# Optimization experiments

Measured on AMD Instinct MI355X. Metric: run time of the kernel, lower is better.

Reference implementation:

```python
import jax, jax.numpy as jnp
import numpy as np

POOL = 7          # cf.pool_size
SR = 2            # roi_align sampling_ratio
LEVELS = [0, 1, 2, 3]
C = 192           # cf.end_filts
HC = 2            # cf.head_classes
RF = 1
N_ROIS = 1000
B = 4


def roi_align_2d(fmap, boxes, batch_inds, pool_size=POOL, sr=SR):
    """Bilinear RoIAlign. fmap [B,C,H,W]; boxes [N,4] = (y1,x1,y2,x2) in fmap pixel coords."""
    _, _, H, W = fmap.shape
    y1, x1, y2, x2 = boxes[:, 0], boxes[:, 1], boxes[:, 2], boxes[:, 3]
    bin_h = jnp.maximum(y2 - y1, 1.0) / pool_size
    bin_w = jnp.maximum(x2 - x1, 1.0) / pool_size
    # sampling offsets within the roi, [pool*sr]
    grid = (jnp.arange(pool_size, dtype=jnp.float32)[:, None]
            + (jnp.arange(sr, dtype=jnp.float32)[None, :] + 0.5) / sr).reshape(-1)
    ys = y1[:, None] + grid[None, :] * bin_h[:, None]   # [N, P*S]
    xs = x1[:, None] + grid[None, :] * bin_w[:, None]   # [N, P*S]
    y = jnp.broadcast_to(ys[:, :, None], (ys.shape[0], ys.shape[1], xs.shape[1]))  # [N,PS,PS]
    x = jnp.broadcast_to(xs[:, None, :], y.shape)
    valid = (y >= -1.0) & (y <= H) & (x >= -1.0) & (x <= W)
    y = jnp.clip(y, 0.0, H - 1)
    x = jnp.clip(x, 0.0, W - 1)
    y0 = jnp.floor(y).astype(jnp.int32)
    x0 = jnp.floor(x).astype(jnp.int32)
    y1i = jnp.minimum(y0 + 1, H - 1)
    x1i = jnp.minimum(x0 + 1, W - 1)
    ly = y - y0
    lx = x - x0
    b = batch_inds[:, None, None]
    f00 = fmap[b, :, y0, x0]    # [N,PS,PS,C]
    f01 = fmap[b, :, y0, x1i]
    f10 = fmap[b, :, y1i, x0]
    f11 = fmap[b, :, y1i, x1i]
    w00 = ((1 - ly) * (1 - lx))[..., None]
    w01 = ((1 - ly) * lx)[..., None]
    w10 = (ly * (1 - lx))[..., None]
    w11 = (ly * lx)[..., None]
    val = (f00 * w00 + f01 * w01 + f10 * w10 + f11 * w11) * valid[..., None]
    n = val.shape[0]
    val = val.reshape(n, pool_size, sr, pool_size, sr, -1).mean(axis=(2, 4))  # [N,P,P,C]
    return jnp.transpose(val, (0, 3, 1, 2))  # [N,C,P,P]


def pyramid_roi_align(fmaps, rois, pool_size=POOL, levels=LEVELS):
    boxes = jax.lax.stop_gradient(rois[:, :4])  # level_boxes.detach() in original
    batch_ix = rois[:, 4].astype(jnp.int32)
    h = boxes[:, 2] - boxes[:, 0]
    w = boxes[:, 3] - boxes[:, 1]
    roi_level = jnp.clip(jnp.round(4.0 + jnp.log2(jnp.sqrt(h * w))),
                         levels[0], levels[-1]).astype(jnp.int32)
    pooled = jnp.zeros((boxes.shape[0], fmaps[0].shape[1], pool_size, pool_size), fmaps[0].dtype)
    for li, lvl in enumerate(levels):
        H, W = fmaps[li].shape[2], fmaps[li].shape[3]
        scale = jnp.asarray([H, W, H, W], jnp.float32)
        p = roi_align_2d(fmaps[li], boxes * scale, batch_ix, pool_size)
        pooled = jnp.where((roi_level == lvl)[:, None, None, None], p, pooled)
    return pooled


def setup_inputs() -> dict:
    key = jax.random.key(0)
    ks = jax.random.split(key, 20)
    fmap0 = jax.random.normal(ks[0], (B, C, 128, 128), jnp.float32)
    fmap1 = jax.random.normal(ks[1], (B, C, 64, 64), jnp.float32)
    fmap2 = jax.random.normal(ks[2], (B, C, 32, 32), jnp.float32)
    fmap3 = jax.random.normal(ks[3], (B, C, 16, 16), jnp.float32)
    # valid normalized rois: (y1,x1,y2,x2,batch_ix)
    cy = jax.random.uniform(ks[4], (N_ROIS,), minval=0.15, maxval=0.85)
    cx = jax.random.uniform(ks[5], (N_ROIS,), minval=0.15, maxval=0.85)
    hh = jax.random.uniform(ks[6], (N_ROIS,), minval=0.02, maxval=0.15)
    hw = jax.random.uniform(ks[7], (N_ROIS,), minval=0.02, maxval=0.15)
    bix = jax.random.randint(ks[8], (N_ROIS,), 0, B).astype(jnp.float32)
    rois = jnp.stack([jnp.clip(cy - hh, 0, 1), jnp.clip(cx - hw, 0, 1),
                      jnp.clip(cy + hh, 0, 1), jnp.clip(cx + hw, 0, 1), bix], axis=1)
    d = C * 4  # 768
    s1 = 1.0 / np.sqrt(C * POOL * POOL)
    s2 = 1.0 / np.sqrt(d)
    params = dict(
        w1=jax.random.normal(ks[9], (d, C, POOL, POOL), jnp.float32) * s1,
        b1=jnp.zeros((d,), jnp.float32),
        w2=jax.random.normal(ks[10], (d, d), jnp.float32) * s2,
        b2=jnp.zeros((d,), jnp.float32),
        w_bbox=jax.random.normal(ks[11], (HC * 4, d), jnp.float32) * s2,
        b_bbox=jnp.zeros((HC * 4,), jnp.float32),
        w_cls=jax.random.normal(ks[12], (HC, d), jnp.float32) * s2,
        b_cls=jnp.zeros((HC,), jnp.float32),
        w_reg=jax.random.normal(ks[13], (HC * RF, d), jnp.float32) * s2,
        b_reg=jnp.zeros((HC * RF,), jnp.float32),
        w_unc=jax.random.normal(ks[14], (HC, d), jnp.float32) * s2,
        b_unc=jnp.zeros((HC,), jnp.float32),
    )
    return dict(fmap0=fmap0, fmap1=fmap1, fmap2=fmap2, fmap3=fmap3, rois=rois, **params)


def reference(fmap0, fmap1, fmap2, fmap3, rois, w1, b1, w2, b2,
              w_bbox, b_bbox, w_cls, b_cls, w_reg, b_reg, w_unc, b_unc):
    x = pyramid_roi_align([fmap0, fmap1, fmap2, fmap3], rois)      # [N,C,7,7]
    x = jax.nn.relu(jnp.einsum('ncij,ocij->no', x, w1) + b1)       # conv1 ks=7 -> 1x1
    x = jax.nn.relu(x @ w2.T + b2)                                 # conv2 1x1
    n = x.shape[0]
    mrcnn_bbox = (x @ w_bbox.T + b_bbox).reshape(n, -1, 4)         # [N,HC,2*dim]
    mrcnn_class_logits = x @ w_cls.T + b_cls                       # [N,HC]
    reg = (x @ w_reg.T + b_reg).reshape(n, -1, RF)
    unc = x @ w_unc.T + b_unc
    mrcnn_regress = jnp.concatenate([reg, unc[..., None]], axis=2)  # [N,HC,RF+1]
    return mrcnn_bbox, mrcnn_class_logits, mrcnn_regress
```

## Files before the change

### kernel.cpp

```cpp
#include <hip/hip_runtime.h>
#include <hip/hip_bf16.h>
#include <cstddef>
#include <cstdint>

typedef __attribute__((ext_vector_type(8))) short short8;
typedef __attribute__((ext_vector_type(16))) float float16;

#define C_CH 192
#define PK   9408
#define D1   768

__device__ __forceinline__ ushort f2bf(float v) {
    return __builtin_bit_cast(unsigned short, __float2bfloat16(v));
}
__device__ __forceinline__ float bf2f(ushort u) {
    return __builtin_bit_cast(float, ((unsigned int)u) << 16);
}

__global__ __launch_bounds__(256) void cvt_bf16_2(
    const float* __restrict__ in1, ushort* __restrict__ out1, int n4_1,
    const float* __restrict__ in2, ushort* __restrict__ out2, int n4_2)
{
    int i = blockIdx.x * 256 + threadIdx.x;
    const float* in; ushort* out;
    if (i < n4_1) { in = in1; out = out1; }
    else          { i -= n4_1; if (i >= n4_2) return; in = in2; out = out2; }
    float4 v = ((const float4*)in)[i];
    ushort4 o;
    o.x = f2bf(v.x); o.y = f2bf(v.y); o.z = f2bf(v.z); o.w = f2bf(v.w);
    ((ushort4*)out)[i] = o;
}

__global__ __launch_bounds__(256) void cvt_bf16(const float* __restrict__ in,
                                                ushort* __restrict__ out, int n4)
{
    int i = blockIdx.x * 256 + threadIdx.x;
    if (i >= n4) return;
    float4 v = ((const float4*)in)[i];
    ushort4 o;
    o.x = f2bf(v.x); o.y = f2bf(v.y); o.z = f2bf(v.z); o.w = f2bf(v.w);
    ((ushort4*)out)[i] = o;
}

__global__ __launch_bounds__(256) void nchw_to_nhwc(
    const float* __restrict__ f0, const float* __restrict__ f1,
    const float* __restrict__ f2, const float* __restrict__ f3,
    ushort* __restrict__ o0, ushort* __restrict__ o1,
    ushort* __restrict__ o2, ushort* __restrict__ o3)
{
    __shared__ float sm[C_CH][33];
    int t = blockIdx.x;
    int b = blockIdx.y;
    const float* in; ushort* out; int HW, hw0;
    if      (t < 512) { in = f0; out = o0; HW = 16384; hw0 = t * 32; }
    else if (t < 640) { in = f1; out = o1; HW = 4096;  hw0 = (t - 512) * 32; }
    else if (t < 672) { in = f2; out = o2; HW = 1024;  hw0 = (t - 640) * 32; }
    else              { in = f3; out = o3; HW = 256;   hw0 = (t - 672) * 32; }

    int tx = threadIdx.x & 31;
    int ty = threadIdx.x >> 5;

    const float* ip = in + (size_t)b * C_CH * HW + hw0;
    #pragma unroll
    for (int c = 0; c < C_CH; c += 8)
        sm[c + ty][tx] = ip[(size_t)(c + ty) * HW + tx];
    __syncthreads();

    ushort* op = out + ((size_t)b * HW + hw0) * C_CH;
    #pragma unroll
    for (int r0 = 0; r0 < 32; r0 += 8) {
        int r = r0 + ty;
        #pragma unroll
        for (int cc = 0; cc < 6; ++cc) {
            int c = cc * 32 + tx;
            op[(size_t)r * C_CH + c] = f2bf(sm[c][r]);
        }
    }
}

__global__ __launch_bounds__(384) void roi_gather(
    const ushort* __restrict__ n0p, const ushort* __restrict__ n1p,
    const ushort* __restrict__ n2p, const ushort* __restrict__ n3p,
    const float* __restrict__ rois, ushort* __restrict__ pooled)
{
    __shared__ int   s_offB[196][4];
    __shared__ float s_w[196][4];
    __shared__ ushort s_out[PK];

    const int n   = blockIdx.x;
    const int tid = threadIdx.x;

    float by1 = rois[n*5+0], bx1 = rois[n*5+1];
    float by2 = rois[n*5+2], bx2 = rois[n*5+3];
    int   b   = (int)rois[n*5+4];

    float hh = by2 - by1, ww = bx2 - bx1;
    int lvl = (int)rintf(4.0f + log2f(sqrtf(hh * ww)));
    lvl = min(max(lvl, 0), 3);

    const ushort* fm; int H;
    if      (lvl == 0) { fm = n0p; H = 128; }
    else if (lvl == 1) { fm = n1p; H = 64;  }
    else if (lvl == 2) { fm = n2p; H = 32;  }
    else               { fm = n3p; H = 16;  }
    float Hf = (float)H;

    float y1p = by1 * Hf, x1p = bx1 * Hf;
    float y2p = by2 * Hf, x2p = bx2 * Hf;
    float bin_h = fmaxf(y2p - y1p, 1.0f) * (1.0f / 7.0f);
    float bin_w = fmaxf(x2p - x1p, 1.0f) * (1.0f / 7.0f);

    uintptr_t bp = (uintptr_t)(fm + (size_t)b * H * H * C_CH);
    unsigned int blo = __builtin_amdgcn_readfirstlane((unsigned int)bp);
    unsigned int bhi = __builtin_amdgcn_readfirstlane((unsigned int)(bp >> 32));
    const char* sbase = (const char*)((((uintptr_t)bhi) << 32) | blo);

    if (tid < 196) {
        int s  = tid;
        int sx = s & 1, sy = (s >> 1) & 1, ij = s >> 2;
        int i = ij / 7, j = ij - i * 7;

        float gy = (float)i + 0.25f + 0.5f * (float)sy;
        float y  = y1p + gy * bin_h;
        bool  vy = (y >= -1.0f) && (y <= Hf);
        float yc = fminf(fmaxf(y, 0.0f), Hf - 1.0f);
        int   y0 = (int)floorf(yc);
        float ly = yc - (float)y0;
        int   y1i = min(y0 + 1, H - 1);

        float gx = (float)j + 0.25f + 0.5f * (float)sx;
        float x  = x1p + gx * bin_w;
        bool  vx = (x >= -1.0f) && (x <= Hf);
        float xc = fminf(fmaxf(x, 0.0f), Hf - 1.0f);
        int   x0 = (int)floorf(xc);
        float lx = xc - (float)x0;
        int   x1i = min(x0 + 1, H - 1);

        float vm = (vy && vx) ? 0.25f : 0.0f;
        s_offB[s][0] = (y0  * H + x0 ) * (C_CH * 2);
        s_offB[s][1] = (y0  * H + x1i) * (C_CH * 2);
        s_offB[s][2] = (y1i * H + x0 ) * (C_CH * 2);
        s_offB[s][3] = (y1i * H + x1i) * (C_CH * 2);
        s_w[s][0] = (1.0f - ly) * (1.0f - lx) * vm;
        s_w[s][1] = (1.0f - ly) * lx * vm;
        s_w[s][2] = ly * (1.0f - lx) * vm;
        s_w[s][3] = ly * lx * vm;
    }
    __syncthreads();

    const int grp = tid / 96;
    const int ci  = tid - grp * 96;
    const int c   = ci * 2;
    const int c4  = ci * 4;
    const int bin_lo = grp * 13;
    const int bin_hi = min(bin_lo + 13, 49);

    for (int bin = bin_lo; bin < bin_hi; ++bin) {
        float a0 = 0.0f, a1 = 0.0f;
        #pragma unroll
        for (int sub = 0; sub < 4; ++sub) {
            int s = bin * 4 + sub;
            #pragma unroll
            for (int tp = 0; tp < 4; ++tp) {
                int ob  = s_offB[s][tp];
                float w = s_w[s][tp];
                unsigned int u = *(const unsigned int*)(sbase + (ob + c4));
                float lo = __builtin_bit_cast(float, u << 16);
                float hi = __builtin_bit_cast(float, u & 0xffff0000u);
                a0 = fmaf(lo, w, a0);
                a1 = fmaf(hi, w, a1);
            }
        }
        s_out[(c + 0) * 49 + bin] = f2bf(a0);
        s_out[(c + 1) * 49 + bin] = f2bf(a1);
    }
    __syncthreads();

    unsigned int* po = (unsigned int*)(pooled + (size_t)n * PK);
    const unsigned int* so = (const unsigned int*)s_out;
    for (int idx = tid; idx < PK / 2; idx += 384) po[idx] = so[idx];
}

__global__ __launch_bounds__(256) void roi_align_nchw(
    const float* __restrict__ f0, const float* __restrict__ f1,
    const float* __restrict__ f2, const float* __restrict__ f3,
    const float* __restrict__ rois, ushort* __restrict__ pooled, int n_rois)
{
    int idx = blockIdx.x * 256 + threadIdx.x;
    if (idx >= n_rois * PK) return;
    int n  = idx / PK;
    int r  = idx - n * PK;
    int c  = r / 49;
    int ij = r - c * 49;
    int i  = ij / 7;
    int j  = ij - i * 7;

    float by1 = rois[n*5+0], bx1 = rois[n*5+1];
    float by2 = rois[n*5+2], bx2 = rois[n*5+3];
    int   b   = (int)rois[n*5+4];

    float hh = by2 - by1, ww = bx2 - bx1;
    int lvl = (int)rintf(4.0f + log2f(sqrtf(hh * ww)));
    lvl = min(max(lvl, 0), 3);

    const float* fmap; int H;
    if      (lvl == 0) { fmap = f0; H = 128; }
    else if (lvl == 1) { fmap = f1; H = 64;  }
    else if (lvl == 2) { fmap = f2; H = 32;  }
    else               { fmap = f3; H = 16;  }
    float Hf = (float)H;

    float y1p = by1 * Hf, x1p = bx1 * Hf;
    float bin_h = fmaxf(by2 * Hf - y1p, 1.0f) * (1.0f / 7.0f);
    float bin_w = fmaxf(bx2 * Hf - x1p, 1.0f) * (1.0f / 7.0f);

    const float* base = fmap + ((size_t)b * C_CH + c) * (size_t)(H * H);

    float acc = 0.0f;
    #pragma unroll
    for (int sy = 0; sy < 2; ++sy) {
        float y  = y1p + ((float)i + 0.25f + 0.5f * (float)sy) * bin_h;
        bool  vy = (y >= -1.0f) && (y <= Hf);
        float yc = fminf(fmaxf(y, 0.0f), Hf - 1.0f);
        int   y0 = (int)floorf(yc);
        float ly = yc - (float)y0;
        int   y1i = min(y0 + 1, H - 1);
        #pragma unroll
        for (int sx = 0; sx < 2; ++sx) {
            float x  = x1p + ((float)j + 0.25f + 0.5f * (float)sx) * bin_w;
            bool  vx = (x >= -1.0f) && (x <= Hf);
            float xc = fminf(fmaxf(x, 0.0f), Hf - 1.0f);
            int   x0 = (int)floorf(xc);
            float lx = xc - (float)x0;
            int   x1i = min(x0 + 1, H - 1);
            if (vy && vx) {
                float v = base[y0 * H + x0 ] * (1.0f - ly) * (1.0f - lx)
                        + base[y0 * H + x1i] * (1.0f - ly) * lx
                        + base[y1i * H + x0 ] * ly * (1.0f - lx)
                        + base[y1i * H + x1i] * ly * lx;
                acc += v;
            }
        }
    }
    pooled[idx] = f2bf(acc * 0.25f);
}

template<int MODE>
__global__ __launch_bounds__(256) void mfma_gemm(
    const ushort* __restrict__ A, const ushort* __restrict__ W,
    const float* __restrict__ bias, void* __restrict__ outp,
    int M, int N, int K, int nkPer, int nkTotal)
{
    __shared__ char ldsA[2][8192];
    __shared__ char ldsB[2][8192];

    const int t    = threadIdx.x;
    const int lane = t & 63;
    const int wave = t >> 6;
    const int wm = wave >> 1, wn = wave & 1;

    const int m0 = blockIdx.y * 64;
    const int n0 = blockIdx.x * 64;
    const int kb = (MODE == 2) ? blockIdx.z * nkPer : 0;
    const int nk = (MODE == 2) ? min(nkPer, nkTotal - kb) : nkPer;

    const int ks   = t & 3;
    const int mrow = t >> 2;
    const int g    = mrow >> 5;
    const int rw   = mrow & 31;
    const int lof0 = ks*2048 + g*1024 + ((     rw) ^ (ks<<2))*16;
    const int lof1 = ks*2048 + g*1024 + ((32 + rw) ^ (ks<<2))*16;

    const int arow = min(m0 + mrow, M-1);
    const int brow = n0 + mrow;
    const ushort* ap = A + (size_t)arow * K + (size_t)kb * 64 + ks*16;
    const ushort* bp = W + (size_t)brow * K + (size_t)kb * 64 + ks*16;

    float4 ra0, ra1, rb0, rb1;
    float4 qa0, qa1, qb0, qb1;

    ra0 = ((const float4*)ap)[0]; ra1 = ((const float4*)ap)[1];
    rb0 = ((const float4*)bp)[0]; rb1 = ((const float4*)bp)[1];
    *(float4*)&ldsA[0][lof0] = ra0; *(float4*)&ldsA[0][lof1] = ra1;
    *(float4*)&ldsB[0][lof0] = rb0; *(float4*)&ldsB[0][lof1] = rb1;
    {
        int k1 = min(1, nk - 1);
        const ushort* ap1 = ap + (size_t)k1 * 64;
        const ushort* bp1 = bp + (size_t)k1 * 64;
        ra0 = ((const float4*)ap1)[0]; ra1 = ((const float4*)ap1)[1];
        rb0 = ((const float4*)bp1)[0]; rb1 = ((const float4*)bp1)[1];
    }
    __syncthreads();

    float16 acc = {};

    for (int kt = 0; kt < nk; ++kt) {
        {
            int k2 = min(kt + 2, nk - 1);
            const ushort* ap2 = ap + (size_t)k2 * 64;
            const ushort* bp2 = bp + (size_t)k2 * 64;
            qa0 = ((const float4*)ap2)[0]; qa1 = ((const float4*)ap2)[1];
            qb0 = ((const float4*)bp2)[0]; qb1 = ((const float4*)bp2)[1];
        }
        if (kt + 1 < nk) {
            char* dA = ldsA[(kt+1)&1]; char* dB = ldsB[(kt+1)&1];
            *(float4*)&dA[lof0] = ra0; *(float4*)&dA[lof1] = ra1;
            *(float4*)&dB[lof0] = rb0; *(float4*)&dB[lof1] = rb1;
        }
        const char* sA = ldsA[kt&1]; const char* sB = ldsB[kt&1];
        #pragma unroll
        for (int s = 0; s < 4; ++s) {
            int ro = s*2048 + (lane ^ (s<<2))*16;
            short8 af = *(const short8*)&sA[wm*1024 + ro];
            short8 bf = *(const short8*)&sB[wn*1024 + ro];
            acc = __builtin_amdgcn_mfma_f32_32x32x16_bf16(af, bf, acc, 0, 0, 0);
        }
        __syncthreads();
        ra0 = qa0; ra1 = qa1; rb0 = qb0; rb1 = qb1;
    }

    const int col   = lane & 31;
    const int rbase = 4 * (lane >> 5);
    const int nG    = n0 + wn*32 + col;

    if (MODE == 2) {
        float* O = (float*)outp + (size_t)blockIdx.z * M * N;
        #pragma unroll
        for (int r = 0; r < 16; ++r) {
            int row = (r & 3) + 8*(r >> 2) + rbase;
            int mG  = m0 + wm*32 + row;
            if (mG < M) O[(size_t)mG * N + nG] = acc[r];
        }
    } else if (MODE == 1) {
        const float bv = bias[nG];
        ushort* O = (ushort*)outp;
        #pragma unroll
        for (int r = 0; r < 16; ++r) {
            int row = (r & 3) + 8*(r >> 2) + rbase;
            int mG  = m0 + wm*32 + row;
            if (mG < M) O[(size_t)mG * N + nG] = f2bf(fmaxf(acc[r] + bv, 0.0f));
        }
    } else {
        const float bv = bias[nG];
        float* O = (float*)outp;
        #pragma unroll
        for (int r = 0; r < 16; ++r) {
            int row = (r & 3) + 8*(r >> 2) + rbase;
            int mG  = m0 + wm*32 + row;
            if (mG < M) O[(size_t)mG * N + nG] = fmaxf(acc[r] + bv, 0.0f);
        }
    }
}

__global__ __launch_bounds__(256) void reduce_relu_bf16(
    const float* __restrict__ P, const float* __restrict__ bias,
    ushort* __restrict__ Y, int MN, int N, int S)
{
    int idx = blockIdx.x * 256 + threadIdx.x;
    if (idx >= MN / 4) return;
    float4 s = ((const float4*)P)[idx];
    for (int k = 1; k < S; ++k) {
        float4 p = ((const float4*)(P + (size_t)k * MN))[idx];
        s.x += p.x; s.y += p.y; s.z += p.z; s.w += p.w;
    }
    int n4 = idx % (N / 4);
    float4 bv = ((const float4*)bias)[n4];
    ushort4 o;
    o.x = f2bf(fmaxf(s.x + bv.x, 0.0f));
    o.y = f2bf(fmaxf(s.y + bv.y, 0.0f));
    o.z = f2bf(fmaxf(s.z + bv.z, 0.0f));
    o.w = f2bf(fmaxf(s.w + bv.w, 0.0f));
    ((ushort4*)Y)[idx] = o;
}

__global__ __launch_bounds__(256) void reduce_heads(
    const float* __restrict__ P2, const float* __restrict__ b2, int S, int MN,
    const float* __restrict__ w_bbox, const float* __restrict__ b_bbox,
    const float* __restrict__ w_cls,  const float* __restrict__ b_cls,
    const float* __restrict__ w_reg,  const float* __restrict__ b_reg,
    const float* __restrict__ w_unc,  const float* __restrict__ b_unc,
    float* __restrict__ out, int n_rois)
{
    __shared__ float zrow[D1];
    const int m   = blockIdx.x;
    const int tid = threadIdx.x;

    const float* Pm = P2 + (size_t)m * D1;
    #pragma unroll
    for (int r = 0; r < 3; ++r) {
        int k = r * 256 + tid;
        float v = Pm[k];
        for (int s = 1; s < S; ++s) v += Pm[(size_t)s * MN + k];
        zrow[k] = fmaxf(v + b2[k], 0.0f);
    }
    __syncthreads();

    const int wave = tid >> 6;
    const int lane = tid & 63;
    for (int o = wave; o < 14; o += 4) {
        const float* w; float bb;
        if      (o < 8)  { w = w_bbox + o * D1;        bb = b_bbox[o]; }
        else if (o < 10) { w = w_cls  + (o - 8) * D1;  bb = b_cls[o - 8]; }
        else if (o < 12) { w = w_reg  + (o - 10) * D1; bb = b_reg[o - 10]; }
        else             { w = w_unc  + (o - 12) * D1; bb = b_unc[o - 12]; }
        float p = 0.0f;
        #pragma unroll
        for (int r = 0; r < 12; ++r) {
            int k = r * 64 + lane;
            p = fmaf(zrow[k], w[k], p);
        }
        #pragma unroll
        for (int d = 32; d >= 1; d >>= 1) p += __shfl_down(p, d, 64);
        if (lane == 0) {
            int off;
            int clsOff = n_rois * 8;
            int regOff = n_rois * 10;
            if      (o < 8)  off = m * 8 + o;
            else if (o < 10) off = clsOff + m * 2 + (o - 8);
            else if (o < 12) off = regOff + m * 4 + (o - 10) * 2;
            else             off = regOff + m * 4 + (o - 12) * 2 + 1;
            out[off] = p + bb;
        }
    }
}

__global__ __launch_bounds__(256) void heads_kernel(
    const float* __restrict__ Z,
    const float* __restrict__ w_bbox, const float* __restrict__ b_bbox,
    const float* __restrict__ w_cls,  const float* __restrict__ b_cls,
    const float* __restrict__ w_reg,  const float* __restrict__ b_reg,
    const float* __restrict__ w_unc,  const float* __restrict__ b_unc,
    float* __restrict__ out, int n_rois)
{
    int idx = blockIdx.x * 256 + threadIdx.x;
    if (idx >= n_rois * 14) return;
    int n = idx / 14;
    int o = idx - n * 14;

    const float* w; float bb;
    if      (o < 8)  { w = w_bbox + o * D1;        bb = b_bbox[o]; }
    else if (o < 10) { w = w_cls  + (o - 8) * D1;  bb = b_cls[o - 8]; }
    else if (o < 12) { w = w_reg  + (o - 10) * D1; bb = b_reg[o - 10]; }
    else             { w = w_unc  + (o - 12) * D1; bb = b_unc[o - 12]; }

    const float* z = Z + (size_t)n * D1;
    float s = bb;
    for (int k = 0; k < D1; k += 4) {
        float4 zv = *(const float4*)(z + k);
        float4 wv = *(const float4*)(w + k);
        s = fmaf(zv.x, wv.x, s);
        s = fmaf(zv.y, wv.y, s);
        s = fmaf(zv.z, wv.z, s);
        s = fmaf(zv.w, wv.w, s);
    }

    int off;
    int clsOff = n_rois * 8;
    int regOff = n_rois * 10;
    if      (o < 8)  off = n * 8 + o;
    else if (o < 10) off = clsOff + n * 2 + (o - 8);
    else if (o < 12) off = regOff + n * 4 + (o - 10) * 2;
    else             off = regOff + n * 4 + (o - 12) * 2 + 1;
    out[off] = s;
}

extern "C" void kernel_launch(void* const* d_in, const int* in_sizes, int n_in,
                              void* d_out, int out_size, void* d_ws, size_t ws_size,
                              hipStream_t stream)
{
    const float* f0   = (const float*)d_in[0];
    const float* f1   = (const float*)d_in[1];
    const float* f2   = (const float*)d_in[2];
    const float* f3   = (const float*)d_in[3];
    const float* rois = (const float*)d_in[4];
    const float* w1   = (const float*)d_in[5];
    const float* b1   = (const float*)d_in[6];
    const float* w2   = (const float*)d_in[7];
    const float* b2   = (const float*)d_in[8];
    const float* w_bbox = (const float*)d_in[9];
    const float* b_bbox = (const float*)d_in[10];
    const float* w_cls  = (const float*)d_in[11];
    const float* b_cls  = (const float*)d_in[12];
    const float* w_reg  = (const float*)d_in[13];
    const float* b_reg  = (const float*)d_in[14];
    const float* w_unc  = (const float*)d_in[15];
    const float* b_unc  = (const float*)d_in[16];
    float* out = (float*)d_out;

    const int n_rois = in_sizes[4] / 5;
    const int B      = in_sizes[0] / (C_CH * 128 * 128);

    const size_t nh0B = (size_t)B * 16384 * C_CH * 2;
    const size_t nh1B = (size_t)B * 4096  * C_CH * 2;
    const size_t nh2B = (size_t)B * 1024  * C_CH * 2;
    const size_t nh3B = (size_t)B * 256   * C_CH * 2;
    const size_t nhAll = nh0B + nh1B + nh2B + nh3B;
    const size_t poolB = (size_t)n_rois * PK * 2;
    const size_t w1Bb  = (size_t)D1 * PK * 2;
    const size_t w2Bb  = (size_t)D1 * D1 * 2;
    const size_t Yb    = (size_t)n_rois * D1 * 2;
    const size_t Zb    = (size_t)n_rois * D1 * 4;
    const size_t smallB = w2Bb + Yb + Zb;

    const size_t needX = nhAll + poolB + smallB;

    char* ws = (char*)d_ws;

    if (ws_size >= needX) {
        const int SPLIT1 = 5;
        const int SPLIT2 = 2;

        ushort* nh0 = (ushort*)ws;
        ushort* nh1 = nh0 + nh0B/2;
        ushort* nh2 = nh1 + nh1B/2;
        ushort* nh3 = nh2 + nh2B/2;
        ushort* w1B = (ushort*)ws;
        float*  P   = (float*)(ws + w1Bb);
        float*  P2  = (float*)ws;
        ushort* pooledB = (ushort*)(ws + nhAll);
        ushort* w2B = (ushort*)(ws + nhAll + poolB);
        ushort* Y   = w2B + w2Bb/2;

        nchw_to_nhwc<<<dim3(680, B), 256, 0, stream>>>(f0, f1, f2, f3,
                                                       nh0, nh1, nh2, nh3);
        roi_gather<<<n_rois, 384, 0, stream>>>(nh0, nh1, nh2, nh3, rois, pooledB);

        {
            int n41 = D1*PK/4, n42 = D1*D1/4;
            cvt_bf16_2<<<(n41 + n42 + 255)/256, 256, 0, stream>>>(
                w1, w1B, n41, w2, w2B, n42);
        }
        {
            int nkTotal = PK / 64;
            int nkPer   = (nkTotal + SPLIT1 - 1) / SPLIT1;
            dim3 grid(D1/64, (n_rois + 63)/64, SPLIT1);
            mfma_gemm<2><<<grid, 256, 0, stream>>>(pooledB, w1B, nullptr, P,
                                                   n_rois, D1, PK, nkPer, nkTotal);
            int MN = n_rois * D1;
            reduce_relu_bf16<<<(MN/4 + 255)/256, 256, 0, stream>>>(P, b1, Y, MN, D1, SPLIT1);
        }
        {
            int nkTotal = D1 / 64;
            int nkPer   = nkTotal / SPLIT2;
            dim3 grid(D1/64, (n_rois + 63)/64, SPLIT2);
            mfma_gemm<2><<<grid, 256, 0, stream>>>(Y, w2B, nullptr, P2,
                                                   n_rois, D1, D1, nkPer, nkTotal);
            int MN = n_rois * D1;
            reduce_heads<<<n_rois, 256, 0, stream>>>(P2, b2, SPLIT2, MN,
                w_bbox, b_bbox, w_cls, b_cls, w_reg, b_reg, w_unc, b_unc, out, n_rois);
        }
    } else {
        ushort* pooledB = (ushort*)ws;
        ushort* w1B = pooledB + poolB/2;
        ushort* w2B = w1B + w1Bb/2;
        ushort* Y   = w2B + w2Bb/2;
        float*  Z   = (float*)((char*)Y + Yb);

        cvt_bf16<<<((D1*PK/4) + 255)/256, 256, 0, stream>>>(w1, w1B, D1*PK/4);
        cvt_bf16<<<((D1*D1/4) + 255)/256, 256, 0, stream>>>(w2, w2B, D1*D1/4);
        {
            int total = n_rois * PK;
            roi_align_nchw<<<(total + 255)/256, 256, 0, stream>>>(
                f0, f1, f2, f3, rois, pooledB, n_rois);
        }
        {
            dim3 grid(D1/64, (n_rois + 63)/64);
            mfma_gemm<1><<<grid, 256, 0, stream>>>(pooledB, w1B, b1, Y,
                                                   n_rois, D1, PK, PK/64, PK/64);
        }
        {
            dim3 grid(D1/64, (n_rois + 63)/64);
            mfma_gemm<0><<<grid, 256, 0, stream>>>(Y, w2B, b2, Z,
                                                   n_rois, D1, D1, D1/64, D1/64);
        }
        heads_kernel<<<(n_rois*14 + 255)/256, 256, 0, stream>>>(
            Z, w_bbox, b_bbox, w_cls, b_cls, w_reg, b_reg, w_unc, b_unc, out, n_rois);
    }
}
```

Measured before the change: 244.3 us.

## Fuse NHWC transpose with weight conversion and split ROI gather across halves

The NCHW-to-NHWC transpose and the fp32-to-bf16 weight conversion now run as one launch, using a new workspace layout so the weight buffers do not alias the NHWC maps. The transpose packs channel pairs into 32-bit words in shared memory and writes them out as coalesced 32-bit stores. ROI gather now uses two 192-thread blocks per ROI, one per channel half, and software-pipelines the 16 gather loads per bin with double-buffered registers. This is meant to cut launch count, speed up the transpose stores, and raise memory-level parallelism in the gather, at the cost of more registers and a larger workspace requirement.

```diff
diff --git a/kernel.cpp b/kernel.cpp
--- a/kernel.cpp
+++ b/kernel.cpp
@@ -12,9 +12,6 @@
 
 __device__ __forceinline__ ushort f2bf(float v) {
     return __builtin_bit_cast(unsigned short, __float2bfloat16(v));
-}
-__device__ __forceinline__ float bf2f(ushort u) {
-    return __builtin_bit_cast(float, ((unsigned int)u) << 16);
 }
 
 __global__ __launch_bounds__(256) void cvt_bf16_2(
@@ -42,15 +39,32 @@
     ((ushort4*)out)[i] = o;
 }
 
-__global__ __launch_bounds__(256) void nchw_to_nhwc(
+__global__ __launch_bounds__(256) void fused_pre(
     const float* __restrict__ f0, const float* __restrict__ f1,
     const float* __restrict__ f2, const float* __restrict__ f3,
     ushort* __restrict__ o0, ushort* __restrict__ o1,
-    ushort* __restrict__ o2, ushort* __restrict__ o3)
-{
-    __shared__ float sm[C_CH][33];
-    int t = blockIdx.x;
-    int b = blockIdx.y;
+    ushort* __restrict__ o2, ushort* __restrict__ o3,
+    const float* __restrict__ w1src, ushort* __restrict__ w1dst, int n41,
+    const float* __restrict__ w2src, ushort* __restrict__ w2dst, int n42,
+    int nTrans)
+{
+    __shared__ unsigned int sm[96][33];
+
+    int bx = blockIdx.x;
+    if (bx >= nTrans) {
+        int i = (bx - nTrans) * 256 + threadIdx.x;
+        const float* in; ushort* out;
+        if (i < n41) { in = w1src; out = w1dst; }
+        else         { i -= n41; if (i >= n42) return; in = w2src; out = w2dst; }
+        float4 v = ((const float4*)in)[i];
+        ushort4 o;
+        o.x = f2bf(v.x); o.y = f2bf(v.y); o.z = f2bf(v.z); o.w = f2bf(v.w);
+        ((ushort4*)out)[i] = o;
+        return;
+    }
+
+    int b = bx / 680;
+    int t = bx - b * 680;
     const float* in; ushort* out; int HW, hw0;
     if      (t < 512) { in = f0; out = o0; HW = 16384; hw0 = t * 32; }
     else if (t < 640) { in = f1; out = o1; HW = 4096;  hw0 = (t - 512) * 32; }
@@ -62,33 +76,61 @@
 
     const float* ip = in + (size_t)b * C_CH * HW + hw0;
     #pragma unroll
-    for (int c = 0; c < C_CH; c += 8)
-        sm[c + ty][tx] = ip[(size_t)(c + ty) * HW + tx];
+    for (int it = 0; it < 12; ++it) {
+        int cp = it * 8 + ty;
+        float v0 = ip[(size_t)(2 * cp)     * HW + tx];
+        float v1 = ip[(size_t)(2 * cp + 1) * HW + tx];
+        sm[cp][tx] = (unsigned int)f2bf(v0) | ((unsigned int)f2bf(v1) << 16);
+    }
     __syncthreads();
 
-    ushort* op = out + ((size_t)b * HW + hw0) * C_CH;
+    unsigned int* op = (unsigned int*)(out + ((size_t)b * HW + hw0) * C_CH);
     #pragma unroll
-    for (int r0 = 0; r0 < 32; r0 += 8) {
-        int r = r0 + ty;
-        #pragma unroll
-        for (int cc = 0; cc < 6; ++cc) {
-            int c = cc * 32 + tx;
-            op[(size_t)r * C_CH + c] = f2bf(sm[c][r]);
-        }
-    }
-}
-
-__global__ __launch_bounds__(384) void roi_gather(
+    for (int it = 0; it < 12; ++it) {
+        int idx = it * 256 + (int)threadIdx.x;
+        int r = idx / 96;
+        int p = idx - r * 96;
+        op[idx] = sm[p][r];
+    }
+}
+
+__device__ __forceinline__ void issue16(
+    const char* sbase, const int (*offB)[4], const float (*wt)[4],
+    int s4, int c4, unsigned int* u, float* w)
+{
+    #pragma unroll
+    for (int k = 0; k < 16; ++k) {
+        int s  = s4 + (k >> 2);
+        int tp = k & 3;
+        u[k] = *(const unsigned int*)(sbase + (offB[s][tp] + c4));
+        w[k] = wt[s][tp];
+    }
+}
+
+__device__ __forceinline__ void comp16(
+    const unsigned int* u, const float* w, float& a0, float& a1)
+{
+    #pragma unroll
+    for (int k = 0; k < 16; ++k) {
+        float lo = __builtin_bit_cast(float, u[k] << 16);
+        float hi = __builtin_bit_cast(float, u[k] & 0xffff0000u);
+        a0 = fmaf(lo, w[k], a0);
+        a1 = fmaf(hi, w[k], a1);
+    }
+}
+
+__global__ __launch_bounds__(192) void roi_gather(
     const ushort* __restrict__ n0p, const ushort* __restrict__ n1p,
     const ushort* __restrict__ n2p, const ushort* __restrict__ n3p,
     const float* __restrict__ rois, ushort* __restrict__ pooled)
 {
-    __shared__ int   s_offB[196][4];
-    __shared__ float s_w[196][4];
-    __shared__ ushort s_out[PK];
-
-    const int n   = blockIdx.x;
-    const int tid = threadIdx.x;
+    __shared__ int    s_offB[196][4];
+    __shared__ float  s_w[196][4];
+    __shared__ ushort s_out[96 * 49];
+
+    const int n    = blockIdx.x >> 1;
+    const int half = blockIdx.x & 1;
+    const int tid  = threadIdx.x;
 
     float by1 = rois[n*5+0], bx1 = rois[n*5+1];
     float by2 = rois[n*5+2], bx2 = rois[n*5+3];
@@ -115,8 +157,7 @@
     unsigned int bhi = __builtin_amdgcn_readfirstlane((unsigned int)(bp >> 32));
     const char* sbase = (const char*)((((uintptr_t)bhi) << 32) | blo);
 
-    if (tid < 196) {
-        int s  = tid;
+    for (int s = tid; s < 196; s += 192) {
         int sx = s & 1, sy = (s >> 1) & 1, ij = s >> 2;
         int i = ij / 7, j = ij - i * 7;
 
@@ -148,37 +189,41 @@
     }
     __syncthreads();
 
-    const int grp = tid / 96;
-    const int ci  = tid - grp * 96;
-    const int c   = ci * 2;
-    const int c4  = ci * 4;
+    const int grp = tid / 48;
+    const int ci  = tid - grp * 48;
+    const int cl  = ci * 2;
+    const int c4  = (half * 96 + cl) * 2;
     const int bin_lo = grp * 13;
     const int bin_hi = min(bin_lo + 13, 49);
 
-    for (int bin = bin_lo; bin < bin_hi; ++bin) {
-        float a0 = 0.0f, a1 = 0.0f;
-        #pragma unroll
-        for (int sub = 0; sub < 4; ++sub) {
-            int s = bin * 4 + sub;
-            #pragma unroll
-            for (int tp = 0; tp < 4; ++tp) {
-                int ob  = s_offB[s][tp];
-                float w = s_w[s][tp];
-                unsigned int u = *(const unsigned int*)(sbase + (ob + c4));
-                float lo = __builtin_bit_cast(float, u << 16);
-                float hi = __builtin_bit_cast(float, u & 0xffff0000u);
-                a0 = fmaf(lo, w, a0);
-                a1 = fmaf(hi, w, a1);
-            }
-        }
-        s_out[(c + 0) * 49 + bin] = f2bf(a0);
-        s_out[(c + 1) * 49 + bin] = f2bf(a1);
+    unsigned int ua[16], ub[16];
+    float        wa[16], wb[16];
+
+    issue16(sbase, s_offB, s_w, bin_lo * 4, c4, ua, wa);
+    int bin = bin_lo;
+    while (true) {
+        if (bin + 1 < bin_hi) issue16(sbase, s_offB, s_w, (bin + 1) * 4, c4, ub, wb);
+        {
+            float a0 = 0.0f, a1 = 0.0f;
+            comp16(ua, wa, a0, a1);
+            s_out[(cl + 0) * 49 + bin] = f2bf(a0);
+            s_out[(cl + 1) * 49 + bin] = f2bf(a1);
+        }
+        if (++bin >= bin_hi) break;
+        if (bin + 1 < bin_hi) issue16(sbase, s_offB, s_w, (bin + 1) * 4, c4, ua, wa);
+        {
+            float a0 = 0.0f, a1 = 0.0f;
+            comp16(ub, wb, a0, a1);
+            s_out[(cl + 0) * 49 + bin] = f2bf(a0);
+            s_out[(cl + 1) * 49 + bin] = f2bf(a1);
+        }
+        if (++bin >= bin_hi) break;
     }
     __syncthreads();
 
-    unsigned int* po = (unsigned int*)(pooled + (size_t)n * PK);
+    unsigned int* po = (unsigned int*)(pooled + (size_t)n * PK + half * 4704);
     const unsigned int* so = (const unsigned int*)s_out;
-    for (int idx = tid; idx < PK / 2; idx += 384) po[idx] = so[idx];
+    for (int idx = tid; idx < 2352; idx += 192) po[idx] = so[idx];
 }
 
 __global__ __launch_bounds__(256) void roi_align_nchw(
@@ -502,14 +547,57 @@
     const size_t Zb    = (size_t)n_rois * D1 * 4;
     const size_t smallB = w2Bb + Yb + Zb;
 
-    const size_t needX = nhAll + poolB + smallB;
+    const int SPLIT1 = 5;
+    const int SPLIT2 = 2;
+
+    const size_t P1b   = (size_t)SPLIT1 * n_rois * D1 * 4;
+    const size_t needX2 = nhAll + poolB + w1Bb + w2Bb + Yb;
+    const size_t needX  = nhAll + poolB + smallB;
 
     char* ws = (char*)d_ws;
 
-    if (ws_size >= needX) {
-        const int SPLIT1 = 5;
-        const int SPLIT2 = 2;
-
+    int n41 = D1*PK/4, n42 = D1*D1/4;
+
+    if (ws_size >= needX2) {
+        ushort* nh0 = (ushort*)ws;
+        ushort* nh1 = nh0 + nh0B/2;
+        ushort* nh2 = nh1 + nh1B/2;
+        ushort* nh3 = nh2 + nh2B/2;
+        ushort* pooledB = (ushort*)(ws + nhAll);
+        ushort* w1B = (ushort*)(ws + nhAll + poolB);
+        ushort* w2B = (ushort*)(ws + nhAll + poolB + w1Bb);
+        ushort* Y   = (ushort*)(ws + nhAll + poolB + w1Bb + w2Bb);
+        float*  P   = (float*)ws;
+        float*  P2  = (float*)(ws + P1b);
+
+        int nTrans = 680 * B;
+        int nCvt   = (n41 + n42 + 255) / 256;
+        fused_pre<<<nTrans + nCvt, 256, 0, stream>>>(
+            f0, f1, f2, f3, nh0, nh1, nh2, nh3,
+            w1, w1B, n41, w2, w2B, n42, nTrans);
+
+        roi_gather<<<2 * n_rois, 192, 0, stream>>>(nh0, nh1, nh2, nh3, rois, pooledB);
+
+        {
+            int nkTotal = PK / 64;
+            int nkPer   = (nkTotal + SPLIT1 - 1) / SPLIT1;
+            dim3 grid(D1/64, (n_rois + 63)/64, SPLIT1);
+            mfma_gemm<2><<<grid, 256, 0, stream>>>(pooledB, w1B, nullptr, P,
+                                                   n_rois, D1, PK, nkPer, nkTotal);
+            int MN = n_rois * D1;
+            reduce_relu_bf16<<<(MN/4 + 255)/256, 256, 0, stream>>>(P, b1, Y, MN, D1, SPLIT1);
+        }
+        {
+            int nkTotal = D1 / 64;
+            int nkPer   = nkTotal / SPLIT2;
+            dim3 grid(D1/64, (n_rois + 63)/64, SPLIT2);
+            mfma_gemm<2><<<grid, 256, 0, stream>>>(Y, w2B, nullptr, P2,
+                                                   n_rois, D1, D1, nkPer, nkTotal);
+            int MN = n_rois * D1;
+            reduce_heads<<<n_rois, 256, 0, stream>>>(P2, b2, SPLIT2, MN,
+                w_bbox, b_bbox, w_cls, b_cls, w_reg, b_reg, w_unc, b_unc, out, n_rois);
+        }
+    } else if (ws_size >= needX) {
         ushort* nh0 = (ushort*)ws;
         ushort* nh1 = nh0 + nh0B/2;
         ushort* nh2 = nh1 + nh1B/2;
@@ -521,15 +609,13 @@
         ushort* w2B = (ushort*)(ws + nhAll + poolB);
         ushort* Y   = w2B + w2Bb/2;
 
-        nchw_to_nhwc<<<dim3(680, B), 256, 0, stream>>>(f0, f1, f2, f3,
-                                                       nh0, nh1, nh2, nh3);
-        roi_gather<<<n_rois, 384, 0, stream>>>(nh0, nh1, nh2, nh3, rois, pooledB);
-
-        {
-            int n41 = D1*PK/4, n42 = D1*D1/4;
-            cvt_bf16_2<<<(n41 + n42 + 255)/256, 256, 0, stream>>>(
-                w1, w1B, n41, w2, w2B, n42);
-        }
+        int nTrans = 680 * B;
+        fused_pre<<<nTrans, 256, 0, stream>>>(
+            f0, f1, f2, f3, nh0, nh1, nh2, nh3,
+            w1, (ushort*)nullptr, 0, w2, (ushort*)nullptr, 0, nTrans);
+        roi_gather<<<2 * n_rois, 192, 0, stream>>>(nh0, nh1, nh2, nh3, rois, pooledB);
+        cvt_bf16_2<<<(n41 + n42 + 255)/256, 256, 0, stream>>>(
+            w1, w1B, n41, w2, w2B, n42);
         {
             int nkTotal = PK / 64;
             int nkPer   = (nkTotal + SPLIT1 - 1) / SPLIT1;
```

After: 228.8 us. -6.3%, faster.
